# Optimization experiments

Measured on AMD Instinct MI355X. Metric: run time of the kernel, lower is better.

## Reference

```python
import jax, jax.numpy as jnp
import numpy as np

B, T, C = 1, 4096, 2048
NH, HS, NQG = 16, 128, 4          # n_head, head_size, n_query_groups (GQA)
Q_PER_KV = NH // NQG              # 4
QKV_DIM = (NH + 2 * NQG) * HS     # 3072
ROT = HS // 2                     # rotary half-dim = 64


def setup_inputs() -> dict:
    key = jax.random.key(0)
    k0, k1, k2 = jax.random.split(key, 3)
    x = jax.random.normal(k0, (B, T, C), dtype=jnp.float32)
    W_attn = jax.random.normal(k1, (QKV_DIM, C), dtype=jnp.float32) * 0.02
    W_proj = jax.random.normal(k2, (C, C), dtype=jnp.float32) * 0.02
    # RoPE cache: cos/sin of shape (T, head_size/2), flash-attn convention
    inv_freq = 1.0 / (10000.0 ** (jnp.arange(0, HS, 2, dtype=jnp.float32) / HS))
    freqs = jnp.arange(T, dtype=jnp.float32)[:, None] * inv_freq[None, :]
    return {"x": x, "cos": jnp.cos(freqs), "sin": jnp.sin(freqs),
            "W_attn": W_attn, "W_proj": W_proj}


def _apply_rope(t, cos, sin):
    # t: (B, T, H, HS); cos/sin: (T, ROT). Non-interleaved (rotate-half) form.
    x1, x2 = t[..., :ROT], t[..., ROT:]
    c = cos[None, :, None, :]
    s = sin[None, :, None, :]
    return jnp.concatenate([x1 * c - x2 * s, x2 * c + x1 * s], axis=-1)


def reference(x, cos, sin, W_attn, W_proj):
    Bx, Tx, Cx = x.shape
    qkv = jnp.einsum('btc,fc->btf', x, W_attn)                 # (B,T,3072)
    qkv = qkv.reshape(Bx, Tx, NQG, Q_PER_KV + 2, HS)
    q = qkv[:, :, :, :Q_PER_KV, :].reshape(Bx, Tx, NH, HS)     # (B,T,16,128)
    k = qkv[:, :, :, Q_PER_KV, :]                              # (B,T,4,128)
    v = qkv[:, :, :, Q_PER_KV + 1, :]                          # (B,T,4,128)
    q = _apply_rope(q, cos, sin)
    k = _apply_rope(k, cos, sin)
    # GQA: expand kv groups to match query heads (repeat_interleave on head dim)
    k = jnp.repeat(k, Q_PER_KV, axis=2)                        # (B,T,16,128)
    v = jnp.repeat(v, Q_PER_KV, axis=2)
    scale = 1.0 / np.sqrt(HS).astype(np.float32)
    scores = jnp.einsum('bthd,bshd->bhts', q, k) * scale       # (B,H,T,T)
    causal = jnp.tril(jnp.ones((Tx, Tx), dtype=bool))
    scores = jnp.where(causal[None, None], scores, jnp.finfo(scores.dtype).min)
    attn = jax.nn.softmax(scores, axis=-1)
    y = jnp.einsum('bhts,bshd->bthd', attn, v).reshape(Bx, Tx, Cx)
    return jnp.einsum('btc,oc->bto', y, W_proj)
```

## Files before the change

kernel.cpp:

```cpp
#include <hip/hip_runtime.h>
#include <hip/hip_bf16.h>

typedef __hip_bfloat16 bf16;
typedef __attribute__((ext_vector_type(8))) short short8;
typedef __attribute__((ext_vector_type(4))) short short4v;
typedef __attribute__((ext_vector_type(4))) float floatx4;

#define T_SEQ 4096
#define C_DIM 2048
#define NHEAD 16
#define HSZ   128
#define NGRP  4

#define MFMA_BF16(A,B,C) __builtin_amdgcn_mfma_f32_16x16x32_bf16((A),(B),(C),0,0,0)

__device__ __forceinline__ void gld_lds16(const bf16* g, bf16* l) {
  __builtin_amdgcn_global_load_lds(
      (__attribute__((address_space(1))) void*)(g),
      (__attribute__((address_space(3))) void*)(l), 16, 0, 0);
}

__global__ void cvt_kernel(const float* __restrict__ src, bf16* __restrict__ dst, long n)
{
  const long i = ((long)blockIdx.x * blockDim.x + threadIdx.x) * 8;
  if (i >= n) return;
  const float4 a = *(const float4*)(src + i);
  const float4 b = *(const float4*)(src + i + 4);
  bf16 tmp[8];
  tmp[0] = __float2bfloat16(a.x); tmp[1] = __float2bfloat16(a.y);
  tmp[2] = __float2bfloat16(a.z); tmp[3] = __float2bfloat16(a.w);
  tmp[4] = __float2bfloat16(b.x); tmp[5] = __float2bfloat16(b.y);
  tmp[6] = __float2bfloat16(b.z); tmp[7] = __float2bfloat16(b.w);
  *(short8*)(dst + i) = *(const short8*)tmp;
}

__global__ __launch_bounds__(256, 2)
void gemm_bt_kernel(const bf16* __restrict__ A, const bf16* __restrict__ B,
                    float* __restrict__ Cf, bf16* __restrict__ Cq,
                    bf16* __restrict__ Ck, bf16* __restrict__ Cvt,
                    int K, int qkv_mode)
{
  __shared__ alignas(16) bf16 As[128 * 64];
  __shared__ alignas(16) bf16 Bs[128 * 64];

  const int t  = threadIdx.x;
  const int w  = t >> 6, l = t & 63;
  const int wr = w >> 1, wc = w & 1;
  const int q4 = l >> 4, ln = l & 15;
  const long bm = (long)blockIdx.y * 128;
  const long bn = (long)blockIdx.x * 128;

  floatx4 acc[4][4] = {};

  const bf16* Ab = A + (bm + t / 8) * (long)K + (t % 8) * 8;
  const bf16* Bb = B + (bn + t / 8) * (long)K + (t % 8) * 8;

  for (int k0 = 0; k0 < K; k0 += 64) {
    __syncthreads();
#pragma unroll
    for (int i = 0; i < 4; ++i) {
      gld_lds16(Ab + (long)i * 32 * K + k0, As + (i * 256 + w * 64) * 8);
      gld_lds16(Bb + (long)i * 32 * K + k0, Bs + (i * 256 + w * 64) * 8);
    }
    __syncthreads();
#pragma unroll
    for (int kk = 0; kk < 64; kk += 32) {
      short8 af[4], bfr[4];
      const int co = kk + q4 * 8;
#pragma unroll
      for (int mi = 0; mi < 4; ++mi)
        af[mi] = *(const short8*)(As + (wr * 64 + mi * 16 + ln) * 64 + co);
#pragma unroll
      for (int ni = 0; ni < 4; ++ni)
        bfr[ni] = *(const short8*)(Bs + (wc * 64 + ni * 16 + ln) * 64 + co);
#pragma unroll
      for (int mi = 0; mi < 4; ++mi)
#pragma unroll
        for (int ni = 0; ni < 4; ++ni)
          acc[mi][ni] = MFMA_BF16(af[mi], bfr[ni], acc[mi][ni]);
    }
  }

  if (!qkv_mode) {
#pragma unroll
    for (int mi = 0; mi < 4; ++mi) {
      const long r0 = bm + wr * 64 + mi * 16 + q4 * 4;
#pragma unroll
      for (int ni = 0; ni < 4; ++ni) {
        const long c = bn + wc * 64 + ni * 16 + ln;
#pragma unroll
        for (int r = 0; r < 4; ++r)
          Cf[(r0 + r) * C_DIM + c] = acc[mi][ni][r];
      }
    }
  } else {
    const int cb = blockIdx.x;
    const int g = cb / 6, slot = cb - g * 6;
    if (slot == 5) {
      bf16* dstv = Cvt + (long)g * HSZ * T_SEQ;
#pragma unroll
      for (int mi = 0; mi < 4; ++mi) {
        const long r0 = bm + wr * 64 + mi * 16 + q4 * 4;
#pragma unroll
        for (int ni = 0; ni < 4; ++ni) {
          const long c = wc * 64 + ni * 16 + ln;
          short4v pk;
#pragma unroll
          for (int r = 0; r < 4; ++r) {
            bf16 v = __float2bfloat16(acc[mi][ni][r]);
            pk[r] = *(short*)&v;
          }
          *(short4v*)(dstv + c * T_SEQ + r0) = pk;
        }
      }
    } else {
      bf16* dst = (slot < 4) ? (Cq + (long)(g * 4 + slot) * T_SEQ * HSZ)
                             : (Ck + (long)g * T_SEQ * HSZ);
#pragma unroll
      for (int mi = 0; mi < 4; ++mi) {
        const long r0 = bm + wr * 64 + mi * 16 + q4 * 4;
#pragma unroll
        for (int ni = 0; ni < 4; ++ni) {
          const long c = wc * 64 + ni * 16 + ln;
#pragma unroll
          for (int r = 0; r < 4; ++r)
            dst[(r0 + r) * HSZ + c] = __float2bfloat16(acc[mi][ni][r]);
        }
      }
    }
  }
}

__global__ void rope_kernel(bf16* __restrict__ Q, bf16* __restrict__ Kb,
                            const float* __restrict__ cs, const float* __restrict__ sn)
{
  const long idx = (long)blockIdx.x * blockDim.x + threadIdx.x;
  const long NQ = (long)NHEAD * T_SEQ * 64;
  bf16* buf; long rem; float qs;
  if (idx < NQ) { buf = Q;  rem = idx;      qs = 0.08838834764831845f * 1.4426950408889634f; }
  else          { buf = Kb; rem = idx - NQ; qs = 1.0f; }
  const int d  = (int)(rem & 63);
  const int tt = (int)((rem >> 6) & (T_SEQ - 1));
  const int hh = (int)(rem >> 18);
  const float c = cs[tt * 64 + d];
  const float s = sn[tt * 64 + d];
  bf16* p = buf + ((long)hh * T_SEQ + tt) * HSZ + d;
  const float x1 = __bfloat162float(p[0]);
  const float x2 = __bfloat162float(p[64]);
  p[0]  = __float2bfloat16((x1 * c - x2 * s) * qs);
  p[64] = __float2bfloat16((x2 * c + x1 * s) * qs);
}

__global__ __launch_bounds__(256, 2)
void attn_kernel(const bf16* __restrict__ Qg, const bf16* __restrict__ Kg,
                 const bf16* __restrict__ Vtg, bf16* __restrict__ Y)
{
  __shared__ alignas(16) bf16 Ks[64][132];
  __shared__ alignas(16) bf16 Vt[128][68];
  __shared__ alignas(16) bf16 Ps[128][68];

  const int h = blockIdx.y;
  const int p = (blockIdx.y < 8) ? blockIdx.x : (31 - blockIdx.x);
  const int g = h >> 2;
  const int t = threadIdx.x;
  const int w = t >> 6, l = t & 63;
  const int q4 = l >> 4, ln = l & 15;

  const bf16* Qh = Qg + (long)h * T_SEQ * HSZ;
  const bf16* Kh = Kg + (long)g * T_SEQ * HSZ;
  const bf16* Vh = Vtg + (long)g * HSZ * T_SEQ;

  const int qbase = p * 128 + w * 32;

  short8 qf[2][4];
#pragma unroll
  for (int mi = 0; mi < 2; ++mi) {
    const long row = qbase + mi * 16 + ln;
#pragma unroll
    for (int ks = 0; ks < 4; ++ks)
      qf[mi][ks] = *(const short8*)(Qh + row * HSZ + ks * 32 + q4 * 8);
  }

  short8 ones_f;
#pragma unroll
  for (int i = 0; i < 8; ++i) ones_f[i] = (ln == 0) ? (short)0x3F80 : (short)0;

  floatx4 acc[2][8] = {};
  floatx4 acc_l[2] = {};

  const int krow = t >> 4, kc = (t & 15) * 8;
  const int vrow = t >> 3, vc = (t & 7) * 8;

  short8 kpre[4], vpre[4];
#pragma unroll
  for (int i = 0; i < 4; ++i) {
    kpre[i] = *(const short8*)(Kh + (long)(krow + 16 * i) * HSZ + kc);
    vpre[i] = *(const short8*)(Vh + (long)(vrow + 32 * i) * T_SEQ + vc);
  }

  const int jmax = 2 * p + 1;
  for (int j = 0; j <= jmax; ++j) {
    const int s0 = j * 64;
#pragma unroll
    for (int i = 0; i < 4; ++i) {
      *(short8*)(&Ks[krow + 16 * i][kc]) = kpre[i];
      *(short8*)(&Vt[vrow + 32 * i][vc]) = vpre[i];
    }
    __syncthreads();
    if (j < jmax) {
      const int s1 = s0 + 64;
#pragma unroll
      for (int i = 0; i < 4; ++i) {
        kpre[i] = *(const short8*)(Kh + (long)(s1 + krow + 16 * i) * HSZ + kc);
        vpre[i] = *(const short8*)(Vh + (long)(vrow + 32 * i) * T_SEQ + s1 + vc);
      }
    }

    floatx4 sacc[2][4] = {};
#pragma unroll
    for (int ks = 0; ks < 4; ++ks) {
      short8 kf[4];
#pragma unroll
      for (int ni = 0; ni < 4; ++ni)
        kf[ni] = *(const short8*)(&Ks[ni * 16 + ln][ks * 32 + q4 * 8]);
#pragma unroll
      for (int mi = 0; mi < 2; ++mi)
#pragma unroll
        for (int ni = 0; ni < 4; ++ni)
          sacc[mi][ni] = MFMA_BF16(qf[mi][ks], kf[ni], sacc[mi][ni]);
    }

#pragma unroll
    for (int mi = 0; mi < 2; ++mi) {
      const int base_m = qbase + mi * 16 + q4 * 4 - s0 - ln;
#pragma unroll
      for (int ni = 0; ni < 4; ++ni)
#pragma unroll
        for (int r = 0; r < 4; ++r) {
          float pv = __builtin_amdgcn_exp2f(sacc[mi][ni][r]);
          if (base_m + r - ni * 16 < 0) pv = 0.f;
          Ps[w * 32 + mi * 16 + q4 * 4 + r][ni * 16 + ln] = __float2bfloat16(pv);
        }
    }

#pragma unroll
    for (int ks = 0; ks < 2; ++ks) {
      short8 pf[2], vf[8];
#pragma unroll
      for (int mi = 0; mi < 2; ++mi)
        pf[mi] = *(const short8*)(&Ps[w * 32 + mi * 16 + ln][ks * 32 + q4 * 8]);
#pragma unroll
      for (int nd = 0; nd < 8; ++nd)
        vf[nd] = *(const short8*)(&Vt[nd * 16 + ln][ks * 32 + q4 * 8]);
#pragma unroll
      for (int mi = 0; mi < 2; ++mi) {
        acc_l[mi] = MFMA_BF16(pf[mi], ones_f, acc_l[mi]);
#pragma unroll
        for (int nd = 0; nd < 8; ++nd)
          acc[mi][nd] = MFMA_BF16(pf[mi], vf[nd], acc[mi][nd]);
      }
    }
    __syncthreads();
  }

#pragma unroll
  for (int mi = 0; mi < 2; ++mi) {
#pragma unroll
    for (int r = 0; r < 4; ++r) {
      const float lv = __shfl(acc_l[mi][r], l & 48, 64);
      const float inv = (lv > 0.f) ? 1.f / lv : 0.f;
      const long tq = qbase + mi * 16 + q4 * 4 + r;
#pragma unroll
      for (int nd = 0; nd < 8; ++nd)
        Y[tq * C_DIM + h * HSZ + nd * 16 + ln] = __float2bfloat16(acc[mi][nd][r] * inv);
    }
  }
}

extern "C" void kernel_launch(void* const* d_in, const int* in_sizes, int n_in,
                              void* d_out, int out_size, void* d_ws, size_t ws_size,
                              hipStream_t stream)
{
  const float* x  = (const float*)d_in[0];
  const float* cs = (const float*)d_in[1];
  const float* sn = (const float*)d_in[2];
  const float* Wa = (const float*)d_in[3];
  const float* Wp = (const float*)d_in[4];
  float* out = (float*)d_out;

  const long nx  = (long)T_SEQ * C_DIM;
  const long nwa = (long)(NHEAD + 2 * NGRP) * HSZ * C_DIM;
  const long nwp = (long)C_DIM * C_DIM;
  const long nqh = (long)NHEAD * T_SEQ * HSZ;
  const long nkg = (long)NGRP * T_SEQ * HSZ;

  const size_t need = (size_t)(nx + nwa + nqh + 2 * nkg + nqh) * sizeof(bf16);
  if (ws_size < need) return;

  bf16* xb  = (bf16*)d_ws;
  bf16* Wab = xb + nx;
  bf16* Q   = Wab + nwa;
  bf16* K   = Q + nqh;
  bf16* Vt  = K + nkg;
  bf16* Y   = Vt + nkg;
  bf16* Wpb = xb;

  cvt_kernel<<<(int)(nx  / 8 / 256), 256, 0, stream>>>(x,  xb,  nx);
  cvt_kernel<<<(int)(nwa / 8 / 256), 256, 0, stream>>>(Wa, Wab, nwa);
  gemm_bt_kernel<<<dim3(24, 32), 256, 0, stream>>>(xb, Wab, nullptr, Q, K, Vt, C_DIM, 1);
  rope_kernel<<<20480, 256, 0, stream>>>(Q, K, cs, sn);
  attn_kernel<<<dim3(32, NHEAD), 256, 0, stream>>>(Q, K, Vt, Y);
  cvt_kernel<<<(int)(nwp / 8 / 256), 256, 0, stream>>>(Wp, Wpb, nwp);
  gemm_bt_kernel<<<dim3(16, 32), 256, 0, stream>>>(Y, Wpb, out, nullptr, nullptr, nullptr, C_DIM, 0);
}
```

Measured before the change: 351.4 us.

## Pair causal q-tiles per block and double-buffer K/V tiles in LDS

```diff
diff --git a/kernel.cpp b/kernel.cpp
--- a/kernel.cpp
+++ b/kernel.cpp
@@ -151,16 +151,15 @@
   p[64] = __float2bfloat16((x2 * c + x1 * s) * qs);
 }
 
-__global__ __launch_bounds__(256, 2)
+__global__ __launch_bounds__(256, 1)
 void attn_kernel(const bf16* __restrict__ Qg, const bf16* __restrict__ Kg,
                  const bf16* __restrict__ Vtg, bf16* __restrict__ Y)
 {
-  __shared__ alignas(16) bf16 Ks[64][132];
-  __shared__ alignas(16) bf16 Vt[128][68];
+  __shared__ alignas(16) bf16 Ks[2][64][132];
+  __shared__ alignas(16) bf16 Vt[2][128][68];
   __shared__ alignas(16) bf16 Ps[128][68];
 
   const int h = blockIdx.y;
-  const int p = (blockIdx.y < 8) ? blockIdx.x : (31 - blockIdx.x);
   const int g = h >> 2;
   const int t = threadIdx.x;
   const int w = t >> 6, l = t & 63;
@@ -170,109 +169,129 @@
   const bf16* Kh = Kg + (long)g * T_SEQ * HSZ;
   const bf16* Vh = Vtg + (long)g * HSZ * T_SEQ;
 
-  const int qbase = p * 128 + w * 32;
-
-  short8 qf[2][4];
-#pragma unroll
-  for (int mi = 0; mi < 2; ++mi) {
-    const long row = qbase + mi * 16 + ln;
-#pragma unroll
-    for (int ks = 0; ks < 4; ++ks)
-      qf[mi][ks] = *(const short8*)(Qh + row * HSZ + ks * 32 + q4 * 8);
-  }
-
-  short8 ones_f;
-#pragma unroll
-  for (int i = 0; i < 8; ++i) ones_f[i] = (ln == 0) ? (short)0x3F80 : (short)0;
-
-  floatx4 acc[2][8] = {};
-  floatx4 acc_l[2] = {};
-
   const int krow = t >> 4, kc = (t & 15) * 8;
   const int vrow = t >> 3, vc = (t & 7) * 8;
 
-  short8 kpre[4], vpre[4];
-#pragma unroll
-  for (int i = 0; i < 4; ++i) {
-    kpre[i] = *(const short8*)(Kh + (long)(krow + 16 * i) * HSZ + kc);
-    vpre[i] = *(const short8*)(Vh + (long)(vrow + 32 * i) * T_SEQ + vc);
-  }
-
-  const int jmax = 2 * p + 1;
-  for (int j = 0; j <= jmax; ++j) {
-    const int s0 = j * 64;
+  short8 ones_f;
+#pragma unroll
+  for (int i = 0; i < 8; ++i) ones_f[i] = (ln == 0) ? (short)0x3F80 : (short)0;
+
+#pragma unroll 1
+  for (int ph = 0; ph < 2; ++ph) {
+    const int p = ph ? (31 - blockIdx.x) : blockIdx.x;
+    const int qbase = p * 128 + w * 32;
+    const int jmax = 2 * p + 1;
+
+    short8 qf[2][4];
+#pragma unroll
+    for (int mi = 0; mi < 2; ++mi) {
+      const long row = qbase + mi * 16 + ln;
+#pragma unroll
+      for (int ks = 0; ks < 4; ++ks)
+        qf[mi][ks] = *(const short8*)(Qh + row * HSZ + ks * 32 + q4 * 8);
+    }
+
+    floatx4 acc[2][8] = {};
+    floatx4 acc_l[2] = {};
+
+    short8 kpre[4], vpre[4];
 #pragma unroll
     for (int i = 0; i < 4; ++i) {
-      *(short8*)(&Ks[krow + 16 * i][kc]) = kpre[i];
-      *(short8*)(&Vt[vrow + 32 * i][vc]) = vpre[i];
+      kpre[i] = *(const short8*)(Kh + (long)(krow + 16 * i) * HSZ + kc);
+      vpre[i] = *(const short8*)(Vh + (long)(vrow + 32 * i) * T_SEQ + vc);
     }
     __syncthreads();
-    if (j < jmax) {
-      const int s1 = s0 + 64;
-#pragma unroll
-      for (int i = 0; i < 4; ++i) {
-        kpre[i] = *(const short8*)(Kh + (long)(s1 + krow + 16 * i) * HSZ + kc);
-        vpre[i] = *(const short8*)(Vh + (long)(vrow + 32 * i) * T_SEQ + s1 + vc);
-      }
-    }
-
-    floatx4 sacc[2][4] = {};
-#pragma unroll
-    for (int ks = 0; ks < 4; ++ks) {
-      short8 kf[4];
-#pragma unroll
-      for (int ni = 0; ni < 4; ++ni)
-        kf[ni] = *(const short8*)(&Ks[ni * 16 + ln][ks * 32 + q4 * 8]);
-#pragma unroll
-      for (int mi = 0; mi < 2; ++mi)
+#pragma unroll
+    for (int i = 0; i < 4; ++i) {
+      *(short8*)(&Ks[0][krow + 16 * i][kc]) = kpre[i];
+      *(short8*)(&Vt[0][vrow + 32 * i][vc]) = vpre[i];
+    }
+#pragma unroll
+    for (int i = 0; i < 4; ++i) {
+      kpre[i] = *(const short8*)(Kh + (long)(64 + krow + 16 * i) * HSZ + kc);
+      vpre[i] = *(const short8*)(Vh + (long)(vrow + 32 * i) * T_SEQ + 64 + vc);
+    }
+
+#pragma unroll 1
+    for (int j = 0; j <= jmax; ++j) {
+      const int s0 = j * 64;
+      const int cur = j & 1;
+      __syncthreads();
+
+      if (j < jmax) {
+        const int nxt = cur ^ 1;
+#pragma unroll
+        for (int i = 0; i < 4; ++i) {
+          *(short8*)(&Ks[nxt][krow + 16 * i][kc]) = kpre[i];
+          *(short8*)(&Vt[nxt][vrow + 32 * i][vc]) = vpre[i];
+        }
+        if (j + 1 < jmax) {
+          const int s2 = s0 + 128;
+#pragma unroll
+          for (int i = 0; i < 4; ++i) {
+            kpre[i] = *(const short8*)(Kh + (long)(s2 + krow + 16 * i) * HSZ + kc);
+            vpre[i] = *(const short8*)(Vh + (long)(vrow + 32 * i) * T_SEQ + s2 + vc);
+          }
+        }
+      }
+
+      floatx4 sacc[2][4] = {};
+#pragma unroll
+      for (int ks = 0; ks < 4; ++ks) {
+        short8 kf[4];
 #pragma unroll
         for (int ni = 0; ni < 4; ++ni)
-          sacc[mi][ni] = MFMA_BF16(qf[mi][ks], kf[ni], sacc[mi][ni]);
+          kf[ni] = *(const short8*)(&Ks[cur][ni * 16 + ln][ks * 32 + q4 * 8]);
+#pragma unroll
+        for (int mi = 0; mi < 2; ++mi)
+#pragma unroll
+          for (int ni = 0; ni < 4; ++ni)
+            sacc[mi][ni] = MFMA_BF16(qf[mi][ks], kf[ni], sacc[mi][ni]);
+      }
+
+#pragma unroll
+      for (int mi = 0; mi < 2; ++mi) {
+        const int base_m = qbase + mi * 16 + q4 * 4 - s0 - ln;
+#pragma unroll
+        for (int ni = 0; ni < 4; ++ni)
+#pragma unroll
+          for (int r = 0; r < 4; ++r) {
+            float pv = __builtin_amdgcn_exp2f(sacc[mi][ni][r]);
+            if (base_m + r - ni * 16 < 0) pv = 0.f;
+            Ps[w * 32 + mi * 16 + q4 * 4 + r][ni * 16 + ln] = __float2bfloat16(pv);
+          }
+      }
+
+#pragma unroll
+      for (int ks = 0; ks < 2; ++ks) {
+        short8 pf[2], vf[8];
+#pragma unroll
+        for (int mi = 0; mi < 2; ++mi)
+          pf[mi] = *(const short8*)(&Ps[w * 32 + mi * 16 + ln][ks * 32 + q4 * 8]);
+#pragma unroll
+        for (int nd = 0; nd < 8; ++nd)
+          vf[nd] = *(const short8*)(&Vt[cur][nd * 16 + ln][ks * 32 + q4 * 8]);
+#pragma unroll
+        for (int mi = 0; mi < 2; ++mi) {
+          acc_l[mi] = MFMA_BF16(pf[mi], ones_f, acc_l[mi]);
+#pragma unroll
+          for (int nd = 0; nd < 8; ++nd)
+            acc[mi][nd] = MFMA_BF16(pf[mi], vf[nd], acc[mi][nd]);
+        }
+      }
     }
 
 #pragma unroll
     for (int mi = 0; mi < 2; ++mi) {
-      const int base_m = qbase + mi * 16 + q4 * 4 - s0 - ln;
-#pragma unroll
-      for (int ni = 0; ni < 4; ++ni)
-#pragma unroll
-        for (int r = 0; r < 4; ++r) {
-          float pv = __builtin_amdgcn_exp2f(sacc[mi][ni][r]);
-          if (base_m + r - ni * 16 < 0) pv = 0.f;
-          Ps[w * 32 + mi * 16 + q4 * 4 + r][ni * 16 + ln] = __float2bfloat16(pv);
-        }
-    }
-
-#pragma unroll
-    for (int ks = 0; ks < 2; ++ks) {
-      short8 pf[2], vf[8];
-#pragma unroll
-      for (int mi = 0; mi < 2; ++mi)
-        pf[mi] = *(const short8*)(&Ps[w * 32 + mi * 16 + ln][ks * 32 + q4 * 8]);
-#pragma unroll
-      for (int nd = 0; nd < 8; ++nd)
-        vf[nd] = *(const short8*)(&Vt[nd * 16 + ln][ks * 32 + q4 * 8]);
-#pragma unroll
-      for (int mi = 0; mi < 2; ++mi) {
-        acc_l[mi] = MFMA_BF16(pf[mi], ones_f, acc_l[mi]);
+#pragma unroll
+      for (int r = 0; r < 4; ++r) {
+        const float lv = __shfl(acc_l[mi][r], l & 48, 64);
+        const float inv = (lv > 0.f) ? 1.f / lv : 0.f;
+        const long tq = qbase + mi * 16 + q4 * 4 + r;
 #pragma unroll
         for (int nd = 0; nd < 8; ++nd)
-          acc[mi][nd] = MFMA_BF16(pf[mi], vf[nd], acc[mi][nd]);
-      }
-    }
-    __syncthreads();
-  }
-
-#pragma unroll
-  for (int mi = 0; mi < 2; ++mi) {
-#pragma unroll
-    for (int r = 0; r < 4; ++r) {
-      const float lv = __shfl(acc_l[mi][r], l & 48, 64);
-      const float inv = (lv > 0.f) ? 1.f / lv : 0.f;
-      const long tq = qbase + mi * 16 + q4 * 4 + r;
-#pragma unroll
-      for (int nd = 0; nd < 8; ++nd)
-        Y[tq * C_DIM + h * HSZ + nd * 16 + ln] = __float2bfloat16(acc[mi][nd][r] * inv);
+          Y[tq * C_DIM + h * HSZ + nd * 16 + ln] = __float2bfloat16(acc[mi][nd][r] * inv);
+      }
     }
   }
 }
@@ -309,7 +328,7 @@
   cvt_kernel<<<(int)(nwa / 8 / 256), 256, 0, stream>>>(Wa, Wab, nwa);
   gemm_bt_kernel<<<dim3(24, 32), 256, 0, stream>>>(xb, Wab, nullptr, Q, K, Vt, C_DIM, 1);
   rope_kernel<<<20480, 256, 0, stream>>>(Q, K, cs, sn);
-  attn_kernel<<<dim3(32, NHEAD), 256, 0, stream>>>(Q, K, Vt, Y);
+  attn_kernel<<<dim3(16, NHEAD), 256, 0, stream>>>(Q, K, Vt, Y);
   cvt_kernel<<<(int)(nwp / 8 / 256), 256, 0, stream>>>(Wp, Wpb, nwp);
   gemm_bt_kernel<<<dim3(16, 32), 256, 0, stream>>>(Y, Wpb, out, nullptr, nullptr, nullptr, C_DIM, 0);
 }
```

Result: slower. 362.7 us (+3.2%).
